# Kernel optimization log

Measured on AMD Instinct MI355X. Metric: run time of the kernel, lower is better.

The kernel has to match this reference:

```python
import jax, jax.numpy as jnp
import numpy as np

B, S, H = 2, 1024, 1024      # batch, seq, hidden_size
FF = 4096                     # shared-expert intermediate_size
E, K, M = 64, 8, 512          # num_experts, top_k, moe_intermediate_size


def setup_inputs() -> dict:
    key = jax.random.key(0)
    ks = jax.random.split(key, 6)
    f32 = jnp.float32
    return {
        "hidden_states": jax.random.normal(ks[0], (B, S, H), f32),
        "Ws1": jax.random.normal(ks[1], (H, FF), f32) * (1.0 / np.sqrt(H)),
        "Ws2": jax.random.normal(ks[2], (FF, H), f32) * (1.0 / np.sqrt(FF)),
        "Wg":  jax.random.normal(ks[3], (H, E), f32) * (1.0 / np.sqrt(H)),
        "W1":  jax.random.normal(ks[4], (E, H, M), f32) * (1.0 / np.sqrt(H)),
        "W2":  jax.random.normal(ks[5], (E, M, H), f32) * (1.0 / np.sqrt(M)),
    }


def reference(hidden_states, Ws1, Ws2, Wg, W1, W2):
    b, s, h = hidden_states.shape
    x = hidden_states.reshape(b * s, h)                 # [T, H]

    # shared expert: SiLU-MLP applied to every token
    shared = jax.nn.silu(x @ Ws1) @ Ws2                 # [T, H]

    # router: top-k gating, softmax over the selected logits only
    logits = x @ Wg                                     # [T, E]
    vals, idx = jax.lax.top_k(logits, K)                # [T, K]
    rw = jax.nn.softmax(vals, axis=-1)                  # [T, K]
    # combine[t, e] = routing weight of expert e for token t (0 if unselected)
    combine = (jax.nn.one_hot(idx, E, dtype=x.dtype) * rw[..., None]).sum(axis=1)  # [T, E]

    # per-expert dense FFN, weighted scatter-add combine (scan keeps memory at O(T*H))
    def step(acc, ew):
        w1, w2, c = ew                                  # [H,M], [M,H], [T]
        y = jax.nn.silu(x @ w1) @ w2                    # [T, H]
        return acc + c[:, None] * y, None

    expert_out, _ = jax.lax.scan(step, jnp.zeros_like(x), (W1, W2, combine.T))

    out = (shared + expert_out).reshape(b, s, h)
    return out, logits.reshape(b, s, E)
```

## Files before the change

kernel.cpp:

```cpp
#include <hip/hip_runtime.h>
#include <cmath>


typedef _Float16 f16;
typedef __attribute__((ext_vector_type(4))) _Float16 f16x4;
typedef __attribute__((ext_vector_type(8))) _Float16 f16x8;
typedef __attribute__((ext_vector_type(4))) float f32x4;

#define NT 2048
#define HD 1024
#define FF 4096
#define NE 64
#define TOPK 8
#define MD 512

constexpr size_t SZ_H1 = (size_t)NT * FF * 2;
constexpr size_t SZ_HX = (size_t)(NT * TOPK + 128) * MD * 2;
constexpr size_t O_H1 = 0;
constexpr size_t O_HX = O_H1 + SZ_H1;
constexpr size_t O_TOPKI = O_HX + SZ_HX;
constexpr size_t O_TOPKW = O_TOPKI + (size_t)NT * TOPK * 4;
constexpr size_t O_COUNTS = O_TOPKW + (size_t)NT * TOPK * 4;
constexpr size_t O_CURSORS = O_COUNTS + 256;
constexpr size_t O_OFFSETS = O_CURSORS + 256;
constexpr size_t O_RTOK = O_OFFSETS + 256;
constexpr size_t O_RW = O_RTOK + (size_t)NT * TOPK * 4;
constexpr size_t O_XH = ((O_RW + (size_t)NT * TOPK * 4 + 255) / 256) * 256;
constexpr size_t O_W1T = O_XH + (size_t)NT * HD * 2;
constexpr size_t O_W2T = O_W1T + (size_t)NE * HD * MD * 2;
constexpr size_t O_WS1T = O_W2T + (size_t)NE * MD * HD * 2;
constexpr size_t O_WS2T = O_WS1T + (size_t)HD * FF * 2;
constexpr size_t WS_NEEDED = O_WS2T + (size_t)FF * HD * 2;

__device__ __forceinline__ void lds16(void* l, const void* g) {
    __builtin_amdgcn_global_load_lds(
        (const __attribute__((address_space(1))) void*)g,
        (__attribute__((address_space(3))) void*)l, 16, 0, 0);
}

__global__ __launch_bounds__(256) void k_router(const float* __restrict__ X,
                                                const float* __restrict__ Wg,
                                                float* __restrict__ logits)
{
    __shared__ float xs[4][HD];
    const int tid = threadIdx.x;
    const int t0 = blockIdx.x * 4;
    #pragma unroll
    for (int i = 0; i < 4; ++i) {
        int f4 = tid + i * 256;
        int row = f4 >> 8;
        int col = (f4 & 255) * 4;
        *(float4*)&xs[row][col] = *(const float4*)&X[(t0 + row) * HD + col];
    }
    __syncthreads();
    const int e = tid & 63, tok = tid >> 6;
    float a0 = 0.f, a1 = 0.f, a2 = 0.f, a3 = 0.f;
    const float* xr = xs[tok];
    for (int h = 0; h < HD; h += 4) {
        a0 += xr[h + 0] * Wg[(h + 0) * NE + e];
        a1 += xr[h + 1] * Wg[(h + 1) * NE + e];
        a2 += xr[h + 2] * Wg[(h + 2) * NE + e];
        a3 += xr[h + 3] * Wg[(h + 3) * NE + e];
    }
    logits[(t0 + tok) * NE + e] = (a0 + a1) + (a2 + a3);
}

__global__ __launch_bounds__(64) void k_topk(const float* __restrict__ logits,
                                             int* __restrict__ topk_idx,
                                             float* __restrict__ topk_w,
                                             int* __restrict__ counts)
{
    const int t = blockIdx.x;
    const int lane = threadIdx.x;
    __shared__ float sval[TOPK];
    __shared__ int sidx[TOPK];
    float cur = logits[t * NE + lane];
    for (int it = 0; it < TOPK; ++it) {
        float v = cur; int id = lane;
        #pragma unroll
        for (int off = 32; off > 0; off >>= 1) {
            float ov = __shfl_xor(v, off, 64);
            int   oi = __shfl_xor(id, off, 64);
            if (ov > v || (ov == v && oi < id)) { v = ov; id = oi; }
        }
        if (lane == 0) { sval[it] = v; sidx[it] = id; }
        if (lane == id) cur = -INFINITY;
    }
    __syncthreads();
    if (lane < TOPK) {
        float m = sval[0];
        float denom = 0.f;
        #pragma unroll
        for (int j = 0; j < TOPK; ++j) denom += expf(sval[j] - m);
        float w = expf(sval[lane] - m) / denom;
        int e = sidx[lane];
        topk_idx[t * TOPK + lane] = e;
        topk_w[t * TOPK + lane] = w;
        atomicAdd(&counts[e], 1);
    }
}

__global__ void k_scan(const int* __restrict__ counts, int* __restrict__ offsets)
{
    if (threadIdx.x == 0) {
        int run = 0;
        for (int e = 0; e < NE; ++e) { offsets[e] = run; run += counts[e]; }
    }
}

__global__ __launch_bounds__(256) void k_route(const int* __restrict__ topk_idx,
                                               const float* __restrict__ topk_w,
                                               const int* __restrict__ offsets,
                                               int* __restrict__ cursors,
                                               int* __restrict__ rtok,
                                               float* __restrict__ rw)
{
    int i = blockIdx.x * 256 + threadIdx.x;
    int e = topk_idx[i];
    int pos = atomicAdd(&cursors[e], 1);
    int slot = offsets[e] + pos;
    rtok[slot] = i >> 3;
    rw[slot] = topk_w[i];
}

__global__ __launch_bounds__(256) void k_cvt_x(const float* __restrict__ X,
                                               f16* __restrict__ Xh)
{
    int i = blockIdx.x * 256 + threadIdx.x;
    float4 v = ((const float4*)X)[i];
    f16x4 h = { (f16)v.x, (f16)v.y, (f16)v.z, (f16)v.w };
    ((f16x4*)Xh)[i] = h;
}

__global__ __launch_bounds__(256) void k_cvt_t(const float* __restrict__ src,
                                               f16* __restrict__ dst,
                                               int K, int N)
{
    const size_t bofs = (size_t)blockIdx.z * K * N;
    src += bofs; dst += bofs;
    const int n0 = blockIdx.x * 64, k0 = blockIdx.y * 64;
    __shared__ f16 t[64][68];
    const int tid = threadIdx.x;
    #pragma unroll
    for (int i = 0; i < 4; ++i) {
        int idx = tid + i * 256;
        int r = idx >> 4, c4 = (idx & 15) * 4;
        float4 v = *(const float4*)&src[(size_t)(k0 + r) * N + n0 + c4];
        f16x4 h = { (f16)v.x, (f16)v.y, (f16)v.z, (f16)v.w };
        *(f16x4*)&t[r][c4] = h;
    }
    __syncthreads();
    #pragma unroll
    for (int i = 0; i < 4; ++i) {
        int idx = tid + i * 256;
        int nr = idx >> 4, kc = (idx & 15) * 4;
        f16x4 o = { t[kc][nr], t[kc + 1][nr], t[kc + 2][nr], t[kc + 3][nr] };
        *(f16x4*)&dst[(size_t)(n0 + nr) * K + k0 + kc] = o;
    }
}


#define GEMM_PREAMBLE                                                        \
    const int tid = threadIdx.x, lane = tid & 63, wave = tid >> 6;           \
    const int wm = (wave >> 1) * 64, wn = (wave & 1) * 64;                   \
    const int fr = lane & 15, q = lane >> 4;                                 \
    const int qs = (q ^ ((fr >> 1) & 3)) * 8;                                \
    const int sr = lane >> 2;                                                \
    const int sc = ((lane & 3) ^ ((lane >> 3) & 3)) * 8;

#define GEMM_LDS                                                             \
    __shared__ alignas(16) f16 As[3][128 * 32];                              \
    __shared__ alignas(16) f16 Bs[3][128 * 32];

#define GEMM_STAGE(si, ofs)                                                  \
    lds16(&As[si][wave * 32 * 32], gA0 + (ofs));                             \
    lds16(&As[si][(wave * 32 + 16) * 32], gA1 + (ofs));                      \
    lds16(&Bs[si][wave * 32 * 32], gB0 + (ofs));                             \
    lds16(&Bs[si][(wave * 32 + 16) * 32], gB1 + (ofs));

#define GEMM_MFMA(ri)                                                        \
    {                                                                        \
        f16x8 af[4], bf[4];                                                  \
        _Pragma("unroll")                                                    \
        for (int i = 0; i < 4; ++i)                                          \
            af[i] = *(const f16x8*)&As[ri][(wm + i * 16 + fr) * 32 + qs];    \
        _Pragma("unroll")                                                    \
        for (int j = 0; j < 4; ++j)                                          \
            bf[j] = *(const f16x8*)&Bs[ri][(wn + j * 16 + fr) * 32 + qs];    \
        _Pragma("unroll")                                                    \
        for (int i = 0; i < 4; ++i)                                          \
            _Pragma("unroll")                                                \
            for (int j = 0; j < 4; ++j)                                      \
                acc[i][j] = __builtin_amdgcn_mfma_f32_16x16x32_f16(          \
                    af[i], bf[j], acc[i][j], 0, 0, 0);                       \
    }

#define GEMM_LOOP(KITERS)                                                    \
    GEMM_STAGE(0, 0)                                                         \
    GEMM_STAGE(1, 32)                                                        \
    _Pragma("unroll")                                                        \
    for (int t = 0; t < (KITERS); ++t) {                                     \
        if (t < (KITERS) - 1)                                                \
            asm volatile("s_waitcnt vmcnt(4)" ::: "memory");                 \
        else                                                                 \
            asm volatile("s_waitcnt vmcnt(0)" ::: "memory");                 \
        __builtin_amdgcn_s_barrier();                                        \
        asm volatile("" ::: "memory");                                       \
        if (t + 2 < (KITERS)) { GEMM_STAGE((t + 2) % 3, (t + 2) * 32) }      \
        GEMM_MFMA(t % 3)                                                     \
    }

__global__ __launch_bounds__(256) void g_shared1(const f16* __restrict__ Xh,
                                                 const f16* __restrict__ Bt,
                                                 f16* __restrict__ H1)
{
    GEMM_LDS
    GEMM_PREAMBLE
    const int m0 = blockIdx.y * 128, n0 = blockIdx.x * 128;
    const f16* gA0 = Xh + (size_t)(m0 + wave * 32 + sr) * HD + sc;
    const f16* gA1 = gA0 + (size_t)16 * HD;
    const f16* gB0 = Bt + (size_t)(n0 + wave * 32 + sr) * HD + sc;
    const f16* gB1 = gB0 + (size_t)16 * HD;

    f32x4 acc[4][4] = {};
    GEMM_LOOP(32)

    #pragma unroll
    for (int i = 0; i < 4; ++i)
        #pragma unroll
        for (int j = 0; j < 4; ++j)
            #pragma unroll
            for (int r = 0; r < 4; ++r) {
                int m = m0 + wm + i * 16 + q * 4 + r;
                int n = n0 + wn + j * 16 + fr;
                float v = acc[i][j][r];
                H1[(size_t)m * FF + n] = (f16)(v / (1.f + expf(-v)));
            }
}

__global__ __launch_bounds__(256) void g_shared2(const f16* __restrict__ H1,
                                                 const f16* __restrict__ Bt,
                                                 float* __restrict__ Out)
{
    GEMM_LDS
    GEMM_PREAMBLE
    const int m0 = blockIdx.y * 128, n0 = blockIdx.x * 128;
    const int kbase = blockIdx.z * (FF / 4);
    const f16* gA0 = H1 + (size_t)(m0 + wave * 32 + sr) * FF + kbase + sc;
    const f16* gA1 = gA0 + (size_t)16 * FF;
    const f16* gB0 = Bt + (size_t)(n0 + wave * 32 + sr) * FF + kbase + sc;
    const f16* gB1 = gB0 + (size_t)16 * FF;

    f32x4 acc[4][4] = {};
    GEMM_LOOP(32)

    #pragma unroll
    for (int i = 0; i < 4; ++i)
        #pragma unroll
        for (int j = 0; j < 4; ++j)
            #pragma unroll
            for (int r = 0; r < 4; ++r) {
                int m = m0 + wm + i * 16 + q * 4 + r;
                int n = n0 + wn + j * 16 + fr;
                atomicAdd(&Out[(size_t)m * HD + n], acc[i][j][r]);
            }
}

__global__ __launch_bounds__(256) void g_exp1(const f16* __restrict__ Xh,
                                              const f16* __restrict__ W1t,
                                              const int* __restrict__ counts,
                                              const int* __restrict__ offsets,
                                              const int* __restrict__ rtok,
                                              f16* __restrict__ Hx)
{
    const int lid = blockIdx.x;
    const int rres = lid & 7;
    const int t2 = lid >> 3;
    const int k = t2 & 63;
    const int g = t2 >> 6;
    const int e = g * 8 + rres;
    const int cnt = counts[e];
    const int mt = (k >> 2) * 128;
    if (mt >= cnt) return;
    const int off = offsets[e];
    const int n0 = (k & 3) * 128;
    const f16* W = W1t + (size_t)e * MD * HD;

    GEMM_LDS
    GEMM_PREAMBLE

    int rm0 = mt + wave * 32 + sr;
    int rm1 = rm0 + 16;
    int s0 = off + (rm0 < cnt ? rm0 : cnt - 1);
    int s1 = off + (rm1 < cnt ? rm1 : cnt - 1);
    const f16* gA0 = Xh + (size_t)rtok[s0] * HD + sc;
    const f16* gA1 = Xh + (size_t)rtok[s1] * HD + sc;
    const f16* gB0 = W + (size_t)(n0 + wave * 32 + sr) * HD + sc;
    const f16* gB1 = gB0 + (size_t)16 * HD;

    f32x4 acc[4][4] = {};
    GEMM_LOOP(32)

    #pragma unroll
    for (int i = 0; i < 4; ++i)
        #pragma unroll
        for (int j = 0; j < 4; ++j)
            #pragma unroll
            for (int r = 0; r < 4; ++r) {
                int m_in = mt + wm + i * 16 + q * 4 + r;
                if (m_in < cnt) {
                    int n = n0 + wn + j * 16 + fr;
                    float v = acc[i][j][r];
                    Hx[(size_t)(off + m_in) * MD + n] = (f16)(v / (1.f + expf(-v)));
                }
            }
}

__global__ __launch_bounds__(256) void g_exp2(const f16* __restrict__ Hx,
                                              const f16* __restrict__ W2t,
                                              const int* __restrict__ counts,
                                              const int* __restrict__ offsets,
                                              const int* __restrict__ rtok,
                                              const float* __restrict__ rw,
                                              float* __restrict__ Out)
{
    const int lid = blockIdx.x;
    const int rres = lid & 7;
    const int t2 = lid >> 3;
    const int k = t2 & 127;
    const int g = t2 >> 7;
    const int e = g * 8 + rres;
    const int cnt = counts[e];
    const int mt = (k >> 3) * 128;
    if (mt >= cnt) return;
    const int off = offsets[e];
    const int n0 = (k & 7) * 128;
    const f16* W = W2t + (size_t)e * HD * MD;

    GEMM_LDS
    GEMM_PREAMBLE

    const f16* gA0 = Hx + (size_t)(off + mt + wave * 32 + sr) * MD + sc;
    const f16* gA1 = gA0 + (size_t)16 * MD;
    const f16* gB0 = W + (size_t)(n0 + wave * 32 + sr) * MD + sc;
    const f16* gB1 = gB0 + (size_t)16 * MD;

    f32x4 acc[4][4] = {};
    GEMM_LOOP(16)

    #pragma unroll
    for (int i = 0; i < 4; ++i)
        #pragma unroll
        for (int r = 0; r < 4; ++r) {
            int m_in = mt + wm + i * 16 + q * 4 + r;
            if (m_in < cnt) {
                int slot = off + m_in;
                int t = rtok[slot];
                float w = rw[slot];
                float* orow = Out + (size_t)t * HD + n0 + wn + fr;
                #pragma unroll
                for (int j = 0; j < 4; ++j)
                    atomicAdd(&orow[j * 16], w * acc[i][j][r]);
            }
        }
}

extern "C" void kernel_launch(void* const* d_in, const int* in_sizes, int n_in,
                              void* d_out, int out_size, void* d_ws, size_t ws_size,
                              hipStream_t stream)
{
    (void)in_sizes; (void)n_in; (void)out_size; (void)ws_size;
    const float* X   = (const float*)d_in[0];
    const float* Ws1 = (const float*)d_in[1];
    const float* Ws2 = (const float*)d_in[2];
    const float* Wg  = (const float*)d_in[3];
    const float* W1  = (const float*)d_in[4];
    const float* W2  = (const float*)d_in[5];
    float* out = (float*)d_out;
    float* logits = out + (size_t)NT * HD;

    char* ws = (char*)d_ws;
    f16*   h1       = (f16*)(ws + O_H1);
    f16*   hx       = (f16*)(ws + O_HX);
    int*   topk_idx = (int*)(ws + O_TOPKI);
    float* topk_w   = (float*)(ws + O_TOPKW);
    int*   counts   = (int*)(ws + O_COUNTS);
    int*   cursors  = (int*)(ws + O_CURSORS);
    int*   offsets  = (int*)(ws + O_OFFSETS);
    int*   rtok     = (int*)(ws + O_RTOK);
    float* rwt      = (float*)(ws + O_RW);
    f16*   xh       = (f16*)(ws + O_XH);
    f16*   w1t      = (f16*)(ws + O_W1T);
    f16*   w2t      = (f16*)(ws + O_W2T);
    f16*   ws1t     = (f16*)(ws + O_WS1T);
    f16*   ws2t     = (f16*)(ws + O_WS2T);

    hipMemsetAsync(counts, 0, 512, stream);

    k_router<<<NT / 4, 256, 0, stream>>>(X, Wg, logits);
    k_topk<<<NT, 64, 0, stream>>>(logits, topk_idx, topk_w, counts);
    k_scan<<<1, 64, 0, stream>>>(counts, offsets);
    k_route<<<NT * TOPK / 256, 256, 0, stream>>>(topk_idx, topk_w, offsets, cursors, rtok, rwt);

    k_cvt_x<<<NT * HD / 1024, 256, 0, stream>>>(X, xh);
    k_cvt_t<<<dim3(FF / 64, HD / 64, 1), 256, 0, stream>>>(Ws1, ws1t, HD, FF);
    k_cvt_t<<<dim3(HD / 64, FF / 64, 1), 256, 0, stream>>>(Ws2, ws2t, FF, HD);
    k_cvt_t<<<dim3(MD / 64, HD / 64, NE), 256, 0, stream>>>(W1, w1t, HD, MD);
    k_cvt_t<<<dim3(HD / 64, MD / 64, NE), 256, 0, stream>>>(W2, w2t, MD, HD);
    hipMemsetAsync(out, 0, (size_t)NT * HD * 4, stream);

    g_shared1<<<dim3(FF / 128, NT / 128), 256, 0, stream>>>(xh, ws1t, h1);
    g_shared2<<<dim3(HD / 128, NT / 128, 4), 256, 0, stream>>>(h1, ws2t, out);
    g_exp1<<<4096, 256, 0, stream>>>(xh, w1t, counts, offsets, rtok, hx);
    g_exp2<<<8192, 256, 0, stream>>>(hx, w2t, counts, offsets, rtok, rwt, out);
}
```

Baseline: 650.3 us.

## Replace atomic output accumulation with per-slot buffers and a deterministic gather kernel

The shared-expert split-K GEMM now writes four fp32 partial planes instead of using atomics. The expert down-projection writes unweighted fp16 rows per routed slot instead of scattering weighted atomics into the output. A new gather kernel sums the partials and the eight routing-weighted expert rows per token, and the output memset is removed. This drops global atomic contention but adds extra write and read traffic (about 32MB fp16 Hy plus 32MB partials), rounds the expert outputs to fp16, and adds one more launch.

```diff
diff --git a/kernel.cpp b/kernel.cpp
--- a/kernel.cpp
+++ b/kernel.cpp
@@ -25,12 +25,16 @@
 constexpr size_t O_OFFSETS = O_CURSORS + 256;
 constexpr size_t O_RTOK = O_OFFSETS + 256;
 constexpr size_t O_RW = O_RTOK + (size_t)NT * TOPK * 4;
-constexpr size_t O_XH = ((O_RW + (size_t)NT * TOPK * 4 + 255) / 256) * 256;
+constexpr size_t O_TSLOT = O_RW + (size_t)NT * TOPK * 4;
+constexpr size_t O_XH = ((O_TSLOT + (size_t)NT * TOPK * 4 + 255) / 256) * 256;
 constexpr size_t O_W1T = O_XH + (size_t)NT * HD * 2;
 constexpr size_t O_W2T = O_W1T + (size_t)NE * HD * MD * 2;
 constexpr size_t O_WS1T = O_W2T + (size_t)NE * MD * HD * 2;
 constexpr size_t O_WS2T = O_WS1T + (size_t)HD * FF * 2;
-constexpr size_t WS_NEEDED = O_WS2T + (size_t)FF * HD * 2;
+constexpr size_t O_HY = O_WS2T + (size_t)FF * HD * 2;
+constexpr size_t SZ_HY = (size_t)(NT * TOPK + 128) * HD * 2;
+constexpr size_t O_S2P = O_HY + SZ_HY;
+constexpr size_t WS_NEEDED = O_S2P + (size_t)4 * NT * HD * 4;
 
 __device__ __forceinline__ void lds16(void* l, const void* g) {
     __builtin_amdgcn_global_load_lds(
@@ -113,14 +117,14 @@
                                                const int* __restrict__ offsets,
                                                int* __restrict__ cursors,
                                                int* __restrict__ rtok,
-                                               float* __restrict__ rw)
+                                               int* __restrict__ tslot)
 {
     int i = blockIdx.x * 256 + threadIdx.x;
     int e = topk_idx[i];
     int pos = atomicAdd(&cursors[e], 1);
     int slot = offsets[e] + pos;
     rtok[slot] = i >> 3;
-    rw[slot] = topk_w[i];
+    tslot[i] = slot;
 }
 
 __global__ __launch_bounds__(256) void k_cvt_x(const float* __restrict__ X,
@@ -240,12 +244,13 @@
 
 __global__ __launch_bounds__(256) void g_shared2(const f16* __restrict__ H1,
                                                  const f16* __restrict__ Bt,
-                                                 float* __restrict__ Out)
+                                                 float* __restrict__ S2p)
 {
     GEMM_LDS
     GEMM_PREAMBLE
     const int m0 = blockIdx.y * 128, n0 = blockIdx.x * 128;
     const int kbase = blockIdx.z * (FF / 4);
+    float* P = S2p + (size_t)blockIdx.z * NT * HD;
     const f16* gA0 = H1 + (size_t)(m0 + wave * 32 + sr) * FF + kbase + sc;
     const f16* gA1 = gA0 + (size_t)16 * FF;
     const f16* gB0 = Bt + (size_t)(n0 + wave * 32 + sr) * FF + kbase + sc;
@@ -262,7 +267,7 @@
             for (int r = 0; r < 4; ++r) {
                 int m = m0 + wm + i * 16 + q * 4 + r;
                 int n = n0 + wn + j * 16 + fr;
-                atomicAdd(&Out[(size_t)m * HD + n], acc[i][j][r]);
+                P[(size_t)m * HD + n] = acc[i][j][r];
             }
 }
 
@@ -320,9 +325,7 @@
                                               const f16* __restrict__ W2t,
                                               const int* __restrict__ counts,
                                               const int* __restrict__ offsets,
-                                              const int* __restrict__ rtok,
-                                              const float* __restrict__ rw,
-                                              float* __restrict__ Out)
+                                              f16* __restrict__ Hy)
 {
     const int lid = blockIdx.x;
     const int rres = lid & 7;
@@ -351,18 +354,49 @@
     #pragma unroll
     for (int i = 0; i < 4; ++i)
         #pragma unroll
-        for (int r = 0; r < 4; ++r) {
-            int m_in = mt + wm + i * 16 + q * 4 + r;
-            if (m_in < cnt) {
-                int slot = off + m_in;
-                int t = rtok[slot];
-                float w = rw[slot];
-                float* orow = Out + (size_t)t * HD + n0 + wn + fr;
-                #pragma unroll
-                for (int j = 0; j < 4; ++j)
-                    atomicAdd(&orow[j * 16], w * acc[i][j][r]);
+        for (int j = 0; j < 4; ++j)
+            #pragma unroll
+            for (int r = 0; r < 4; ++r) {
+                int m_in = mt + wm + i * 16 + q * 4 + r;
+                if (m_in < cnt) {
+                    int n = n0 + wn + j * 16 + fr;
+                    Hy[(size_t)(off + m_in) * HD + n] = (f16)acc[i][j][r];
+                }
             }
-        }
+}
+
+__global__ __launch_bounds__(256) void k_gather(const float* __restrict__ S2p,
+                                                const f16* __restrict__ Hy,
+                                                const int* __restrict__ tslot,
+                                                const float* __restrict__ tw,
+                                                float* __restrict__ Out)
+{
+    const int t = blockIdx.x;
+    const int tid = threadIdx.x;
+    __shared__ int ss[TOPK];
+    __shared__ float sw[TOPK];
+    if (tid < TOPK) {
+        ss[tid] = tslot[t * TOPK + tid];
+        sw[tid] = tw[t * TOPK + tid];
+    }
+    __syncthreads();
+    const int h = tid * 4;
+    float4 a = *(const float4*)&S2p[(size_t)t * HD + h];
+    #pragma unroll
+    for (int z = 1; z < 4; ++z) {
+        float4 b = *(const float4*)&S2p[(size_t)z * NT * HD + (size_t)t * HD + h];
+        a.x += b.x; a.y += b.y; a.z += b.z; a.w += b.w;
+    }
+    #pragma unroll
+    for (int kk = 0; kk < TOPK; ++kk) {
+        f16x4 y = *(const f16x4*)&Hy[(size_t)ss[kk] * HD + h];
+        float w = sw[kk];
+        a.x += w * (float)y[0];
+        a.y += w * (float)y[1];
+        a.z += w * (float)y[2];
+        a.w += w * (float)y[3];
+    }
+    *(float4*)&Out[(size_t)t * HD + h] = a;
 }
 
 extern "C" void kernel_launch(void* const* d_in, const int* in_sizes, int n_in,
@@ -388,29 +422,31 @@
     int*   cursors  = (int*)(ws + O_CURSORS);
     int*   offsets  = (int*)(ws + O_OFFSETS);
     int*   rtok     = (int*)(ws + O_RTOK);
-    float* rwt      = (float*)(ws + O_RW);
+    int*   tslot    = (int*)(ws + O_TSLOT);
     f16*   xh       = (f16*)(ws + O_XH);
     f16*   w1t      = (f16*)(ws + O_W1T);
     f16*   w2t      = (f16*)(ws + O_W2T);
     f16*   ws1t     = (f16*)(ws + O_WS1T);
     f16*   ws2t     = (f16*)(ws + O_WS2T);
+    f16*   hy       = (f16*)(ws + O_HY);
+    float* s2p      = (float*)(ws + O_S2P);
 
     hipMemsetAsync(counts, 0, 512, stream);
 
     k_router<<<NT / 4, 256, 0, stream>>>(X, Wg, logits);
     k_topk<<<NT, 64, 0, stream>>>(logits, topk_idx, topk_w, counts);
     k_scan<<<1, 64, 0, stream>>>(counts, offsets);
-    k_route<<<NT * TOPK / 256, 256, 0, stream>>>(topk_idx, topk_w, offsets, cursors, rtok, rwt);
+    k_route<<<NT * TOPK / 256, 256, 0, stream>>>(topk_idx, topk_w, offsets, cursors, rtok, tslot);
 
     k_cvt_x<<<NT * HD / 1024, 256, 0, stream>>>(X, xh);
     k_cvt_t<<<dim3(FF / 64, HD / 64, 1), 256, 0, stream>>>(Ws1, ws1t, HD, FF);
     k_cvt_t<<<dim3(HD / 64, FF / 64, 1), 256, 0, stream>>>(Ws2, ws2t, FF, HD);
     k_cvt_t<<<dim3(MD / 64, HD / 64, NE), 256, 0, stream>>>(W1, w1t, HD, MD);
     k_cvt_t<<<dim3(HD / 64, MD / 64, NE), 256, 0, stream>>>(W2, w2t, MD, HD);
-    hipMemsetAsync(out, 0, (size_t)NT * HD * 4, stream);
 
     g_shared1<<<dim3(FF / 128, NT / 128), 256, 0, stream>>>(xh, ws1t, h1);
-    g_shared2<<<dim3(HD / 128, NT / 128, 4), 256, 0, stream>>>(h1, ws2t, out);
+    g_shared2<<<dim3(HD / 128, NT / 128, 4), 256, 0, stream>>>(h1, ws2t, s2p);
     g_exp1<<<4096, 256, 0, stream>>>(xh, w1t, counts, offsets, rtok, hx);
-    g_exp2<<<8192, 256, 0, stream>>>(hx, w2t, counts, offsets, rtok, rwt, out);
-}
+    g_exp2<<<8192, 256, 0, stream>>>(hx, w2t, counts, offsets, hy);
+    k_gather<<<NT, 256, 0, stream>>>(s2p, hy, tslot, topk_w, out);
+}
```

Result: faster. 612.4 us (-5.8%).
